# Optimization experiments

Hardware: AMD Instinct MI355X
Metric: run time of the kernel (lower is better)

## Reference

```python
import jax, jax.numpy as jnp
import numpy as np
import math

KORD = 3          # Chebyshev order K
N = 512           # num_of_vertices
D = 64            # d_model // 2
DM = 128          # d_model
NEG_SLOPE = 0.01  # torch F.leaky_relu default


def _cheb_coef_matrix(K):
    # coe[i] = 2/(K+1) * sum_j relu(temp)[j] * T_i(x_j), x_j = cos((K-j+0.5)pi/(K+1))
    xs = [math.cos((K - j + 0.5) * math.pi / (K + 1)) for j in range(K + 1)]
    M = np.array([[math.cos(i * math.acos(xj)) for xj in xs] for i in range(K + 1)],
                 dtype=np.float32)
    return (2.0 / (K + 1)) * M


def setup_inputs() -> dict:
    key = jax.random.key(0)
    ks = jax.random.split(key, 12)
    B, L = 4, 32
    sc_n = 1.0 / math.sqrt(N)
    sc_d = 1.0 / math.sqrt(D)
    return {
        "x":    jax.random.normal(ks[0], (B, L, N), jnp.float32),
        "adj":  jax.random.normal(ks[1], (N, N), jnp.float32) * sc_n,
        "Wp":   jax.random.normal(ks[2], (1, D), jnp.float32),            # project: Linear(1, D)
        "bp":   jnp.zeros((D,), jnp.float32),
        "Ksa":  jax.random.normal(ks[3], (N, N), jnp.float32) * sc_n,     # Spatial_Attention.K
        "Vsa":  jax.random.normal(ks[4], (N, N), jnp.float32) * sc_n,     # Spatial_Attention.V
        "bsa":  jax.random.normal(ks[5], (1, N, N), jnp.float32) * sc_n,  # Spatial_Attention.b
        "temp": jnp.ones((KORD + 1,), jnp.float32),                       # init fill_(1.0)
        "W1":   jax.random.normal(ks[6], (D, D), jnp.float32) * sc_d,     # Theta1_
        "b1":   jnp.zeros((D,), jnp.float32),
        "Wl":   jax.random.normal(ks[7], (N * D, DM), jnp.float32) / math.sqrt(N * D),  # linear_
        "bl":   jnp.zeros((DM,), jnp.float32),
    }


def _leaky(v):
    return jnp.where(v >= 0, v, NEG_SLOPE * v)


def reference(x, adj, Wp, bp, Ksa, Vsa, bsa, temp, W1, b1, Wl, bl):
    B, L, _ = x.shape
    # project: (B,L,N,1) @ (1,D) + bias -> (B,L,N,D)   (dropout = eval identity)
    h = x[..., None] * Wp[0] + bp

    # Chebyshev coefficients from relu(temp)
    coe = jnp.asarray(_cheb_coef_matrix(KORD)) @ jax.nn.relu(temp)  # (K+1,)

    # Chebyshev recursion on graph: Tx_{k+1} = 2*adj@Tx_k - Tx_{k-1}
    Tx0 = h
    Tx1 = jnp.einsum('nm,blmd->blnd', adj, h)
    A_x = coe[0] / 2 * Tx0 + coe[1] * Tx1
    for i in range(2, KORD + 1):
        Tx2 = 2 * jnp.einsum('nm,blmd->blnd', adj, Tx1) - Tx0
        A_x = A_x + coe[i] * Tx2
        Tx0, Tx1 = Tx1, Tx2

    # Spatial attention: softmax(V @ tanh(x (Kx)^T + b))
    Kx = jnp.einsum('nm,blmd->blnd', Ksa, h)                 # K @ x
    product = jnp.einsum('blnd,blmd->blnm', h, Kx)           # x @ (Kx)^T
    score = jnp.einsum('nm,blmc->blnc', Vsa, jnp.tanh(product + bsa[0]))
    SA = jax.nn.softmax(score, axis=-1)                      # (B,L,N,N)

    S_x = jnp.einsum('blnm,blmd->blnd', SA, h)
    g = A_x + S_x
    g = _leaky(jnp.einsum('blnd,de->blne', g, W1) + b1)      # Theta1_ + leaky_relu
    g = g.reshape(B, L, N * D)
    return _leaky(g @ Wl + bl)                               # linear_ + leaky_relu -> (B,L,DM)
```

## Files before the change

kernel.cpp:

```cpp
#include <hip/hip_runtime.h>
#include <math.h>

#define KORD 3
#ifndef M_PI
#define M_PI 3.14159265358979323846
#endif

typedef __attribute__((ext_vector_type(8))) __bf16 bf16x8;
typedef __attribute__((ext_vector_type(4))) float  f32x4;

__device__ __forceinline__ float leaky_(float v){ return v >= 0.f ? v : 0.01f*v; }

__device__ __forceinline__ float tanh_fast(float x){
  float xc = fminf(fmaxf(x, -10.f), 10.f);
  float t = __expf(2.f*xc);
  return (t - 1.f) * __builtin_amdgcn_rcpf(t + 1.f);
}

__device__ __forceinline__ f32x4 mfma16(bf16x8 a, bf16x8 b, f32x4 c){
  return __builtin_amdgcn_mfma_f32_16x16x32_bf16(a, b, c, 0, 0, 0);
}

__device__ __forceinline__ void gll16(const __bf16* g, __bf16* l){
  __builtin_amdgcn_global_load_lds(
      (__attribute__((address_space(1))) void*)(g),
      (__attribute__((address_space(3))) void*)(l), 16, 0, 0);
}

__global__ void k_coe(const float* __restrict__ temp, float* __restrict__ coe){
  if (threadIdx.x == 0 && blockIdx.x == 0){
    for (int i = 0; i <= KORD; ++i){
      float acc = 0.f;
      for (int j = 0; j <= KORD; ++j){
        double th = ((double)(KORD - j) + 0.5) * M_PI / (double)(KORD + 1);
        float t = temp[j]; t = t > 0.f ? t : 0.f;
        acc += t * (float)cos((double)i * th);
      }
      acc *= 2.f / (float)(KORD + 1);
      if (i >= 1 && fabsf(acc) < 1e-6f) acc = 0.f;
      coe[i] = acc;
    }
  }
}

__global__ __launch_bounds__(256) void k_cvt(const float* __restrict__ in,
                                             __bf16* __restrict__ out, int n){
  int i = blockIdx.x*256 + threadIdx.x;
  if (i < n) out[i] = (__bf16)in[i];
}

__global__ __launch_bounds__(256) void k_cvt_swz(const float* __restrict__ in,
                                                 __bf16* __restrict__ out){
  int i = blockIdx.x*256 + threadIdx.x;
  int r = i >> 9, c = i & 511;
  out[(size_t)r*512 + (c ^ ((r & 7) << 3))] = (__bf16)in[i];
}

__global__ __launch_bounds__(256) void k_w1t(const float* __restrict__ W1,
                                             __bf16* __restrict__ W1t){
  int t = threadIdx.x;
  for (int i = 0; i < 16; ++i){
    int e4 = i*256 + t;
    int e = e4 >> 6, d = e4 & 63;
    W1t[e*64 + d] = (__bf16)W1[d*64 + e];
  }
}

__global__ __launch_bounds__(256) void k_wlt(const float* __restrict__ Wl,
                                             __bf16* __restrict__ Wlt){
  __shared__ float Ls[64][65];
  int k0 = blockIdx.x*64, o0 = blockIdx.y*64;
  int t = threadIdx.x;
  for (int i = 0; i < 16; ++i){
    int e = i*256 + t; int r = e >> 6, c = e & 63;
    Ls[r][c] = Wl[(size_t)(k0 + r)*128 + o0 + c];
  }
  __syncthreads();
  for (int i = 0; i < 16; ++i){
    int e = i*256 + t; int r = e >> 6, c = e & 63;
    Wlt[(size_t)(o0 + r)*32768 + k0 + c] = (__bf16)Ls[c][r];
  }
}

__global__ __launch_bounds__(256) void k_bsat(const float* __restrict__ bsa,
                                              __bf16* __restrict__ bsaTb){
  __shared__ float Ls[64][65];
  int n0 = blockIdx.x*64, m0 = blockIdx.y*64;
  int t = threadIdx.x;
  for (int i = 0; i < 16; ++i){
    int e = i*256 + t; int r = e >> 6, c = e & 63;
    Ls[r][c] = bsa[(size_t)(n0 + r)*512 + m0 + c];
  }
  __syncthreads();
  for (int i = 0; i < 16; ++i){
    int e = i*256 + t; int r = e >> 6, c = e & 63;
    bsaTb[(size_t)(m0 + r)*512 + n0 + c] = (__bf16)Ls[c][r];
  }
}

__global__ __launch_bounds__(256) void k_embed2(const float* __restrict__ x,
    const float* __restrict__ Wp, const float* __restrict__ bp,
    __bf16* __restrict__ Ht, __bf16* __restrict__ Hnd, __bf16* __restrict__ Htsw){
  __shared__ float Ls[64][65];
  int cs = blockIdx.x, n0 = blockIdx.y*64;
  int t = threadIdx.x;
  for (int i = 0; i < 16; ++i){
    int e = i*256 + t; int d = e >> 6, nn = e & 63;
    float v = x[cs*512 + n0 + nn]*Wp[d] + bp[d];
    Ls[d][nn] = v;
    Ht[(size_t)(cs*64 + d)*512 + n0 + nn] = (__bf16)v;
    Htsw[(size_t)(cs*64 + d)*512 + ((n0 + nn) ^ ((d & 7) << 3))] = (__bf16)v;
  }
  __syncthreads();
  for (int i = 0; i < 16; ++i){
    int e = i*256 + t; int nn = e >> 6, d = e & 63;
    Hnd[((size_t)cs*512 + n0 + nn)*64 + d] = (__bf16)Ls[d][nn];
  }
}

__global__ __launch_bounds__(256) void k_combo(const __bf16* __restrict__ Ht,
    const __bf16* __restrict__ T1t, const __bf16* __restrict__ T2t,
    const __bf16* __restrict__ T3t, const __bf16* __restrict__ SXnd,
    const float* __restrict__ coe, __bf16* __restrict__ Gnd){
  __shared__ float Ls[64][65];
  int cs = blockIdx.x, n0 = blockIdx.y*64;
  int t = threadIdx.x;
  float c0 = coe[0]*0.5f, c1 = coe[1], c2 = coe[2], c3 = coe[3];
  for (int i = 0; i < 16; ++i){
    int e = i*256 + t; int d = e >> 6, nn = e & 63;
    size_t idx = (size_t)(cs*64 + d)*512 + n0 + nn;
    float v = c0*(float)Ht[idx];
    if (c1 != 0.f) v += c1*(float)T1t[idx];
    if (c2 != 0.f) v += c2*(float)T2t[idx];
    if (c3 != 0.f) v += c3*(float)T3t[idx];
    Ls[d][nn] = v;
  }
  __syncthreads();
  for (int i = 0; i < 16; ++i){
    int e = i*256 + t; int nn = e >> 6, d = e & 63;
    size_t oidx = ((size_t)cs*512 + n0 + nn)*64 + d;
    Gnd[oidx] = (__bf16)(Ls[d][nn] + (float)SXnd[oidx]);
  }
}

template<int BM, int BN, int WM, int WN, int EPI, bool SWZ>
__global__ __launch_bounds__(256) void gbt(
    const __bf16* __restrict__ A, size_t aB, int lda,
    const __bf16* __restrict__ B, size_t bB, int ldb,
    const void*  __restrict__ E, size_t eB,
    void* __restrict__ C, size_t cB, int ldc, int K, int gx, int gy,
    const float* __restrict__ gate, int gateCnt){
  if (gate){
    bool anyNZ = false;
    for (int i = 0; i < gateCnt; ++i) anyNZ |= (gate[i] != 0.f);
    if (!anyNZ) return;
  }
  constexpr int WTM = BM/WM, WTN = BN/WN;
  constexpr int FM = WTM/16, FN = WTN/16;
  constexpr int LDK = 72;
  constexpr bool RPK = (EPI == 2 && BM == 128 && BN == 128);
  __shared__ __bf16 SMEM[BM*LDK + BN*LDK];
  __bf16* As = SMEM;
  __bf16* Bs = SMEM + BM*LDK;
  const int tid = threadIdx.x;
  const int wave = tid >> 6, lane = tid & 63;
  const int wm = wave % WM, wn = wave / WM;
  int bx, by, bz;
  if (SWZ){
    int id = blockIdx.x;
    int xcd = id & 7, j = id >> 3;
    int tiles = gx*gy;
    int tile = j % tiles, sin = j / tiles;
    bz = xcd + 8*sin; bx = tile % gx; by = tile / gx;
  } else { bx = blockIdx.x; by = blockIdx.y; bz = blockIdx.z; }
  const int m0 = bx*BM, n0 = by*BN;
  const __bf16* Ab = A + (size_t)bz*aB + (size_t)m0*lda;
  const __bf16* Bb = B + (size_t)bz*bB + (size_t)n0*ldb;
  f32x4 acc[FM][FN] = {};
  for (int k0 = 0; k0 < K; k0 += 64){
    __syncthreads();
    constexpr int AIT = BM*64/(256*8);
#pragma unroll
    for (int i = 0; i < AIT; ++i){
      int e = i*256 + tid; int r = e >> 3, c = (e & 7)*8;
      *(float4*)&As[r*LDK + c] = *(const float4*)&Ab[(size_t)r*lda + k0 + c];
    }
    constexpr int BIT = BN*64/(256*8);
#pragma unroll
    for (int i = 0; i < BIT; ++i){
      int e = i*256 + tid; int r = e >> 3, c = (e & 7)*8;
      *(float4*)&Bs[r*LDK + c] = *(const float4*)&Bb[(size_t)r*ldb + k0 + c];
    }
    __syncthreads();
#pragma unroll
    for (int ks = 0; ks < 2; ++ks){
      bf16x8 af[FM], bfr[FN];
      const int ko = ks*32 + (lane >> 4)*8;
#pragma unroll
      for (int i = 0; i < FM; ++i)
        af[i] = *(const bf16x8*)&As[(wm*WTM + i*16 + (lane & 15))*LDK + ko];
#pragma unroll
      for (int j = 0; j < FN; ++j)
        bfr[j] = *(const bf16x8*)&Bs[(wn*WTN + j*16 + (lane & 15))*LDK + ko];
#pragma unroll
      for (int i = 0; i < FM; ++i)
#pragma unroll
        for (int j = 0; j < FN; ++j)
          acc[i][j] = mfma16(af[i], bfr[j], acc[i][j]);
    }
  }
  const int lr = (lane >> 4)*4, lc = lane & 15;
  __bf16* Cb = (__bf16*)C + (size_t)bz*cB;
  if constexpr (RPK){
    const __bf16* Eb = (const __bf16*)E;
    __syncthreads();
    __bf16* R = SMEM;
#pragma unroll
    for (int i = 0; i < FM; ++i)
#pragma unroll
      for (int j = 0; j < FN; ++j)
#pragma unroll
        for (int r = 0; r < 4; ++r){
          int row = wm*64 + i*16 + lr + r;
          int col = wn*64 + j*16 + lc;
          float v = tanh_fast(acc[i][j][r] + (float)Eb[(size_t)(m0 + row)*512 + (n0 + col)]);
          R[row*136 + col] = (__bf16)v;
        }
    __syncthreads();
#pragma unroll
    for (int it = 0; it < 8; ++it){
      int q = it*256 + tid; int row = q >> 4, ch = q & 15;
      *(bf16x8*)&Cb[(size_t)(m0 + row)*ldc + (n0 + ((ch*8) ^ ((row & 7) << 3)))] =
          *(const bf16x8*)&R[row*136 + ch*8];
    }
    return;
  }
  float*  Cf = (float*)C  + (size_t)bz*cB;
  const __bf16* Zb = (const __bf16*)E + (size_t)bz*eB;
  const float*  Ef = (const float*)E;
  const __bf16* Eb = (const __bf16*)E;
#pragma unroll
  for (int i = 0; i < FM; ++i){
    int row = m0 + wm*WTM + i*16 + lr;
#pragma unroll
    for (int j = 0; j < FN; ++j){
      int col = n0 + wn*WTN + j*16 + lc;
#pragma unroll
      for (int r = 0; r < 4; ++r){
        float v = acc[i][j][r];
        size_t idx = (size_t)(row + r)*ldc + col;
        if (EPI == 0){ Cb[idx] = (__bf16)v; }
        else if (EPI == 1){ Cb[idx] = (__bf16)(2.f*v - (float)Zb[idx]); }
        else if (EPI == 2){ Cb[(size_t)(row + r)*ldc + (col ^ (((row + r) & 7) << 3))] =
                              (__bf16)tanh_fast(v + (float)Eb[(size_t)(row + r)*512 + col]); }
        else if (EPI == 3){ Cf[idx] = v; }
        else if (EPI == 5){ float tt = v + Ef[col]; Cb[idx] = (__bf16)(tt >= 0.f ? tt : 0.01f*tt); }
      }
    }
  }
}

template<bool SWZ>
__global__ __launch_bounds__(256) void k_flash(
    const __bf16* __restrict__ Vsab,
    const __bf16* __restrict__ Pt,
    const __bf16* __restrict__ Htsw,
    __bf16* __restrict__ SXnd){
  __shared__ __bf16 VaL[2][4096];
  __shared__ __bf16 PbL[2][4096];
  __shared__ __bf16 Ps[64*72];
  __shared__ __bf16 Hb[4096];
  __shared__ float rs2[2][64];
  const int tid = threadIdx.x, wave = tid >> 6, lane = tid & 63;
  const int wm = wave & 1, wn = wave >> 1;
  const int lr = (lane >> 4)*4, lc = lane & 15;
  int np0, z;
  if (SWZ){
    int id = blockIdx.x;
    int xcd = id & 7, j = id >> 3;
    int tile = j & 7, sin = j >> 3;
    z = xcd + 8*sin; np0 = tile*64;
  } else { np0 = blockIdx.x*64; z = blockIdx.y; }
  const __bf16* Vb = Vsab + (size_t)np0*512;
  const __bf16* Pz = Pt + (size_t)z*262144;
  const __bf16* Hz = Htsw + (size_t)z*32768;
  const int srow = lane >> 3;
  const int scol = (lane & 7)*8;
  auto stage = [&](int buf, int c0, int k0){
#pragma unroll
    for (int rr = 0; rr < 2; ++rr){
      int rb = (rr*4 + wave)*8;
      gll16(Vb + (size_t)(rb + srow)*512 + k0 + scol, &VaL[buf][(rr*4 + wave)*512]);
      gll16(Pz + (size_t)(c0 + rb + srow)*512 + k0 + scol, &PbL[buf][(rr*4 + wave)*512]);
    }
  };
  const int kx = (lc & 7) << 3;
  f32x4 acc_sx[2][2] = {};
  float rowp[8] = {};
  stage(0, 0, 0);
  __syncthreads();
  for (int c0i = 0; c0i < 8; ++c0i){
    const int c0 = c0i*64;
    f32x4 acc_s[2][2] = {};
    for (int k0i = 0; k0i < 8; ++k0i){
      const int t = c0i*8 + k0i;
      const int cur = t & 1;
      if (t < 63){
        int nt = t + 1;
        stage(cur ^ 1, (nt >> 3)*64, (nt & 7)*64);
      }
      if (k0i == 1){
#pragma unroll
        for (int rr = 0; rr < 2; ++rr){
          int rb = (rr*4 + wave)*8;
          gll16(Hz + (size_t)(rb + srow)*512 + c0 + scol, &Hb[(rr*4 + wave)*512]);
        }
      }
#pragma unroll
      for (int ks = 0; ks < 2; ++ks){
        const int kox = (ks*32 + (lane >> 4)*8) ^ kx;
        bf16x8 a0 = *(const bf16x8*)&VaL[cur][(wm*32 +  0 + lc)*64 + kox];
        bf16x8 a1 = *(const bf16x8*)&VaL[cur][(wm*32 + 16 + lc)*64 + kox];
        bf16x8 b0 = *(const bf16x8*)&PbL[cur][(wn*32 +  0 + lc)*64 + kox];
        bf16x8 b1 = *(const bf16x8*)&PbL[cur][(wn*32 + 16 + lc)*64 + kox];
        acc_s[0][0] = mfma16(a0, b0, acc_s[0][0]);
        acc_s[0][1] = mfma16(a0, b1, acc_s[0][1]);
        acc_s[1][0] = mfma16(a1, b0, acc_s[1][0]);
        acc_s[1][1] = mfma16(a1, b1, acc_s[1][1]);
      }
      __syncthreads();
    }
#pragma unroll
    for (int i = 0; i < 2; ++i)
#pragma unroll
      for (int j = 0; j < 2; ++j)
#pragma unroll
        for (int rr = 0; rr < 4; ++rr){
          float e = __expf(fminf(acc_s[i][j][rr], 30.f));
          rowp[i*4 + rr] += e;
          Ps[(wm*32 + i*16 + lr + rr)*72 + wn*32 + j*16 + lc] = (__bf16)e;
        }
    __syncthreads();
#pragma unroll
    for (int ks = 0; ks < 2; ++ks){
      const int ko = ks*32 + (lane >> 4)*8;
      const int kox = ko ^ kx;
      bf16x8 p0 = *(const bf16x8*)&Ps[(wm*32 +  0 + lc)*72 + ko];
      bf16x8 p1 = *(const bf16x8*)&Ps[(wm*32 + 16 + lc)*72 + ko];
      bf16x8 h0 = *(const bf16x8*)&Hb[(wn*32 +  0 + lc)*64 + kox];
      bf16x8 h1 = *(const bf16x8*)&Hb[(wn*32 + 16 + lc)*64 + kox];
      acc_sx[0][0] = mfma16(p0, h0, acc_sx[0][0]);
      acc_sx[0][1] = mfma16(p0, h1, acc_sx[0][1]);
      acc_sx[1][0] = mfma16(p1, h0, acc_sx[1][0]);
      acc_sx[1][1] = mfma16(p1, h1, acc_sx[1][1]);
    }
  }
#pragma unroll
  for (int s = 0; s < 8; ++s){
    float v = rowp[s];
    v += __shfl_xor(v, 1, 64); v += __shfl_xor(v, 2, 64);
    v += __shfl_xor(v, 4, 64); v += __shfl_xor(v, 8, 64);
    rowp[s] = v;
  }
  __syncthreads();
  if ((lane & 15) == 0){
#pragma unroll
    for (int i = 0; i < 2; ++i)
#pragma unroll
      for (int rr = 0; rr < 4; ++rr)
        rs2[wn][wm*32 + i*16 + lr + rr] = rowp[i*4 + rr];
  }
  __syncthreads();
#pragma unroll
  for (int i = 0; i < 2; ++i)
#pragma unroll
    for (int rr = 0; rr < 4; ++rr){
      int row = wm*32 + i*16 + lr + rr;
      float inv = __builtin_amdgcn_rcpf(rs2[0][row] + rs2[1][row]);
#pragma unroll
      for (int j = 0; j < 2; ++j){
        int col = wn*32 + j*16 + lc;
        SXnd[((size_t)z*512 + np0 + row)*64 + col] = (__bf16)(acc_sx[i][j][rr]*inv);
      }
    }
}

__global__ __launch_bounds__(256) void k_final2(
    const float* __restrict__ part, const float* __restrict__ bl,
    float* __restrict__ out){
  int idx = blockIdx.x*256 + threadIdx.x;
  int o = idx & 127;
  float acc = bl[o];
#pragma unroll 8
  for (int p = 0; p < 128; ++p) acc += part[(size_t)p*16384 + idx];
  out[idx] = leaky_(acc);
}

extern "C" void kernel_launch(void* const* d_in, const int* in_sizes, int n_in,
                              void* d_out, int out_size, void* d_ws, size_t ws_size,
                              hipStream_t stream){
  const float* x    = (const float*)d_in[0];
  const float* adj  = (const float*)d_in[1];
  const float* Wp   = (const float*)d_in[2];
  const float* bp   = (const float*)d_in[3];
  const float* Ksa  = (const float*)d_in[4];
  const float* Vsa  = (const float*)d_in[5];
  const float* bsa  = (const float*)d_in[6];
  const float* temp = (const float*)d_in[7];
  const float* W1   = (const float*)d_in[8];
  const float* b1   = (const float*)d_in[9];
  const float* Wl   = (const float*)d_in[10];
  const float* bl   = (const float*)d_in[11];
  float* out = (float*)d_out;

  char* ws = (char*)d_ws;
  size_t off = 0;
  auto alloc = [&](size_t bytes){ void* p = ws + off; off += (bytes + 255) & ~(size_t)255; return p; };
  float*  coe  = (float*)alloc(64);
  __bf16* G2b  = (__bf16*)alloc((size_t)128*32768*2);
  __bf16* Wlt  = (__bf16*)alloc((size_t)128*32768*2);
  float*  part = (float*)alloc((size_t)128*16384*4);
  __bf16* bsaTb= (__bf16*)alloc((size_t)512*512*2);
  __bf16* adjb = (__bf16*)alloc((size_t)512*512*2);
  __bf16* Ksab = (__bf16*)alloc((size_t)512*512*2);
  __bf16* Vsab = (__bf16*)alloc((size_t)512*512*2);
  __bf16* W1t  = (__bf16*)alloc((size_t)64*64*2);
  const size_t fixedOff = off;

  int CH = 128;
  while (CH > 2){
    size_t need = fixedOff + (size_t)CH*(9*65536 + 524288) + 65536;
    if (need <= ws_size) break;
    CH >>= 1;
  }
  __bf16* Ht   = (__bf16*)alloc((size_t)CH*65536);
  __bf16* Htsw = (__bf16*)alloc((size_t)CH*65536);
  __bf16* T1t  = (__bf16*)alloc((size_t)CH*65536);
  __bf16* T2t  = (__bf16*)alloc((size_t)CH*65536);
  __bf16* T3t  = (__bf16*)alloc((size_t)CH*65536);
  __bf16* KXnd = (__bf16*)alloc((size_t)CH*65536);
  __bf16* Hnd  = (__bf16*)alloc((size_t)CH*65536);
  __bf16* SXnd = (__bf16*)alloc((size_t)CH*65536);
  __bf16* Gnd  = (__bf16*)alloc((size_t)CH*65536);
  __bf16* Pt   = (__bf16*)alloc((size_t)CH*524288);

  const bool swz = (CH % 8) == 0;

  k_coe<<<1, 64, 0, stream>>>(temp, coe);
  k_cvt<<<1024, 256, 0, stream>>>(adj, adjb, 512*512);
  k_cvt<<<1024, 256, 0, stream>>>(Ksa, Ksab, 512*512);
  k_cvt_swz<<<1024, 256, 0, stream>>>(Vsa, Vsab);
  k_w1t<<<1, 256, 0, stream>>>(W1, W1t);
  k_wlt<<<dim3(512,2), 256, 0, stream>>>(Wl, Wlt);
  k_bsat<<<dim3(8,8), 256, 0, stream>>>(bsa, bsaTb);

  for (int s0 = 0; s0 < 128; s0 += CH){
    k_embed2<<<dim3(CH,8), 256, 0, stream>>>(x + (size_t)s0*512, Wp, bp, Ht, Hnd, Htsw);
    gbt<64,128,2,2,0,false><<<dim3(CH,4,1), 256, 0, stream>>>(Ht, 0, 512, adjb, 0, 512, nullptr, 0, T1t, 0, 512, 512, 0, 0, coe+1, 3);
    gbt<64,128,2,2,1,false><<<dim3(CH,4,1), 256, 0, stream>>>(T1t, 0, 512, adjb, 0, 512, Ht, 0, T2t, 0, 512, 512, 0, 0, coe+2, 2);
    gbt<64,128,2,2,1,false><<<dim3(CH,4,1), 256, 0, stream>>>(T2t, 0, 512, adjb, 0, 512, T1t, 0, T3t, 0, 512, 512, 0, 0, coe+3, 1);
    gbt<64,64,2,2,0,false><<<dim3(8,1,CH), 256, 0, stream>>>(Ksab, 0, 512, Ht, 32768, 512,
                                                             nullptr, 0, KXnd, 32768, 64, 512, 0, 0, nullptr, 0);
    if (swz)
      gbt<128,128,2,2,2,true><<<dim3(16*CH), 256, 0, stream>>>(KXnd, 32768, 64, Hnd, 32768, 64,
                                                               bsaTb, 0, Pt, 262144, 512, 64, 4, 4, nullptr, 0);
    else
      gbt<128,128,2,2,2,false><<<dim3(4,4,CH), 256, 0, stream>>>(KXnd, 32768, 64, Hnd, 32768, 64,
                                                                 bsaTb, 0, Pt, 262144, 512, 64, 0, 0, nullptr, 0);
    if (swz)
      k_flash<true><<<dim3(8*CH), 256, 0, stream>>>(Vsab, Pt, Htsw, SXnd);
    else
      k_flash<false><<<dim3(8,CH), 256, 0, stream>>>(Vsab, Pt, Htsw, SXnd);
    k_combo<<<dim3(CH,8), 256, 0, stream>>>(Ht, T1t, T2t, T3t, SXnd, coe, Gnd);
    gbt<64,64,2,2,5,false><<<dim3(8,1,CH), 256, 0, stream>>>(Gnd, 32768, 64, W1t, 0, 64,
                                                             b1, 0, G2b + (size_t)s0*32768, 32768, 64, 64, 0, 0, nullptr, 0);
  }

  gbt<128,128,2,2,3,false><<<dim3(1,1,128), 256, 0, stream>>>(G2b, 256, 32768, Wlt, 256, 32768,
                                                              nullptr, 0, part, 16384, 128, 256, 0, 0, nullptr, 0);
  k_final2<<<dim3(64), 256, 0, stream>>>(part, bl, out);
}
```

Baseline: 196.4 us.

## Triple-buffer flash kernel loads and read H directly from global memory

The flash kernel moves from double to triple buffering for the V and P tiles, keeping two stages in flight and using explicit vmcnt waits with a single barrier per step instead of __syncthreads. The H operand is now loaded straight from global memory into registers rather than staged through a swizzled LDS buffer. That lets the embed kernel drop the swizzled Htsw copy and frees one workspace buffer. In exchange it relies on hand-counted vmcnt values, which could race if the count of outstanding loads is wrong, and the H reads from global are uncoalesced.

```diff
diff --git a/kernel.cpp b/kernel.cpp
--- a/kernel.cpp
+++ b/kernel.cpp
@@ -100,7 +100,7 @@
 
 __global__ __launch_bounds__(256) void k_embed2(const float* __restrict__ x,
     const float* __restrict__ Wp, const float* __restrict__ bp,
-    __bf16* __restrict__ Ht, __bf16* __restrict__ Hnd, __bf16* __restrict__ Htsw){
+    __bf16* __restrict__ Ht, __bf16* __restrict__ Hnd){
   __shared__ float Ls[64][65];
   int cs = blockIdx.x, n0 = blockIdx.y*64;
   int t = threadIdx.x;
@@ -109,7 +109,6 @@
     float v = x[cs*512 + n0 + nn]*Wp[d] + bp[d];
     Ls[d][nn] = v;
     Ht[(size_t)(cs*64 + d)*512 + n0 + nn] = (__bf16)v;
-    Htsw[(size_t)(cs*64 + d)*512 + ((n0 + nn) ^ ((d & 7) << 3))] = (__bf16)v;
   }
   __syncthreads();
   for (int i = 0; i < 16; ++i){
@@ -264,12 +263,11 @@
 __global__ __launch_bounds__(256) void k_flash(
     const __bf16* __restrict__ Vsab,
     const __bf16* __restrict__ Pt,
-    const __bf16* __restrict__ Htsw,
+    const __bf16* __restrict__ Ht,
     __bf16* __restrict__ SXnd){
-  __shared__ __bf16 VaL[2][4096];
-  __shared__ __bf16 PbL[2][4096];
+  __shared__ __bf16 VaL[3][4096];
+  __shared__ __bf16 PbL[3][4096];
   __shared__ __bf16 Ps[64*72];
-  __shared__ __bf16 Hb[4096];
   __shared__ float rs2[2][64];
   const int tid = threadIdx.x, wave = tid >> 6, lane = tid & 63;
   const int wm = wave & 1, wn = wave >> 1;
@@ -283,10 +281,10 @@
   } else { np0 = blockIdx.x*64; z = blockIdx.y; }
   const __bf16* Vb = Vsab + (size_t)np0*512;
   const __bf16* Pz = Pt + (size_t)z*262144;
-  const __bf16* Hz = Htsw + (size_t)z*32768;
+  const __bf16* Hz = Ht + (size_t)z*32768;
   const int srow = lane >> 3;
   const int scol = (lane & 7)*8;
-  auto stage = [&](int buf, int c0, int k0){
+  auto stageVP = [&](int buf, int c0, int k0){
 #pragma unroll
     for (int rr = 0; rr < 2; ++rr){
       int rb = (rr*4 + wave)*8;
@@ -297,38 +295,41 @@
   const int kx = (lc & 7) << 3;
   f32x4 acc_sx[2][2] = {};
   float rowp[8] = {};
-  stage(0, 0, 0);
-  __syncthreads();
+  stageVP(0, 0, 0);
+  stageVP(1, 0, 64);
+  int cur = 0;
   for (int c0i = 0; c0i < 8; ++c0i){
     const int c0 = c0i*64;
     f32x4 acc_s[2][2] = {};
+#pragma unroll
     for (int k0i = 0; k0i < 8; ++k0i){
-      const int t = c0i*8 + k0i;
-      const int cur = t & 1;
-      if (t < 63){
-        int nt = t + 1;
-        stage(cur ^ 1, (nt >> 3)*64, (nt & 7)*64);
-      }
-      if (k0i == 1){
-#pragma unroll
-        for (int rr = 0; rr < 2; ++rr){
-          int rb = (rr*4 + wave)*8;
-          gll16(Hz + (size_t)(rb + srow)*512 + c0 + scol, &Hb[(rr*4 + wave)*512]);
-        }
-      }
+      if (k0i == 7){
+        if (c0i == 7) asm volatile("s_waitcnt vmcnt(0)" ::: "memory");
+        else          asm volatile("s_waitcnt vmcnt(4)" ::: "memory");
+      } else {
+        asm volatile("s_waitcnt vmcnt(4)" ::: "memory");
+      }
+      __builtin_amdgcn_s_barrier();
+      const __bf16* Vc = VaL[cur];
+      const __bf16* Pc = PbL[cur];
 #pragma unroll
       for (int ks = 0; ks < 2; ++ks){
         const int kox = (ks*32 + (lane >> 4)*8) ^ kx;
-        bf16x8 a0 = *(const bf16x8*)&VaL[cur][(wm*32 +  0 + lc)*64 + kox];
-        bf16x8 a1 = *(const bf16x8*)&VaL[cur][(wm*32 + 16 + lc)*64 + kox];
-        bf16x8 b0 = *(const bf16x8*)&PbL[cur][(wn*32 +  0 + lc)*64 + kox];
-        bf16x8 b1 = *(const bf16x8*)&PbL[cur][(wn*32 + 16 + lc)*64 + kox];
+        bf16x8 a0 = *(const bf16x8*)&Vc[(wm*32 +  0 + lc)*64 + kox];
+        bf16x8 a1 = *(const bf16x8*)&Vc[(wm*32 + 16 + lc)*64 + kox];
+        bf16x8 b0 = *(const bf16x8*)&Pc[(wn*32 +  0 + lc)*64 + kox];
+        bf16x8 b1 = *(const bf16x8*)&Pc[(wn*32 + 16 + lc)*64 + kox];
         acc_s[0][0] = mfma16(a0, b0, acc_s[0][0]);
         acc_s[0][1] = mfma16(a0, b1, acc_s[0][1]);
         acc_s[1][0] = mfma16(a1, b0, acc_s[1][0]);
         acc_s[1][1] = mfma16(a1, b1, acc_s[1][1]);
       }
-      __syncthreads();
+      int nt = c0i*8 + k0i + 2;
+      if (nt < 64){
+        int bufn = cur + 2; if (bufn >= 3) bufn -= 3;
+        stageVP(bufn, (nt >> 3) << 6, (nt & 7) << 6);
+      }
+      cur = (cur == 2) ? 0 : cur + 1;
     }
 #pragma unroll
     for (int i = 0; i < 2; ++i)
@@ -340,19 +341,24 @@
           rowp[i*4 + rr] += e;
           Ps[(wm*32 + i*16 + lr + rr)*72 + wn*32 + j*16 + lc] = (__bf16)e;
         }
-    __syncthreads();
+    bf16x8 h0k[2], h1k[2];
 #pragma unroll
     for (int ks = 0; ks < 2; ++ks){
       const int ko = ks*32 + (lane >> 4)*8;
-      const int kox = ko ^ kx;
+      h0k[ks] = *(const bf16x8*)&Hz[(size_t)(wn*32 +  0 + lc)*512 + c0 + ko];
+      h1k[ks] = *(const bf16x8*)&Hz[(size_t)(wn*32 + 16 + lc)*512 + c0 + ko];
+    }
+    asm volatile("s_waitcnt lgkmcnt(0)" ::: "memory");
+    __builtin_amdgcn_s_barrier();
+#pragma unroll
+    for (int ks = 0; ks < 2; ++ks){
+      const int ko = ks*32 + (lane >> 4)*8;
       bf16x8 p0 = *(const bf16x8*)&Ps[(wm*32 +  0 + lc)*72 + ko];
       bf16x8 p1 = *(const bf16x8*)&Ps[(wm*32 + 16 + lc)*72 + ko];
-      bf16x8 h0 = *(const bf16x8*)&Hb[(wn*32 +  0 + lc)*64 + kox];
-      bf16x8 h1 = *(const bf16x8*)&Hb[(wn*32 + 16 + lc)*64 + kox];
-      acc_sx[0][0] = mfma16(p0, h0, acc_sx[0][0]);
-      acc_sx[0][1] = mfma16(p0, h1, acc_sx[0][1]);
-      acc_sx[1][0] = mfma16(p1, h0, acc_sx[1][0]);
-      acc_sx[1][1] = mfma16(p1, h1, acc_sx[1][1]);
+      acc_sx[0][0] = mfma16(p0, h0k[ks], acc_sx[0][0]);
+      acc_sx[0][1] = mfma16(p0, h1k[ks], acc_sx[0][1]);
+      acc_sx[1][0] = mfma16(p1, h0k[ks], acc_sx[1][0]);
+      acc_sx[1][1] = mfma16(p1, h1k[ks], acc_sx[1][1]);
     }
   }
 #pragma unroll
@@ -429,12 +435,11 @@
 
   int CH = 128;
   while (CH > 2){
-    size_t need = fixedOff + (size_t)CH*(9*65536 + 524288) + 65536;
+    size_t need = fixedOff + (size_t)CH*(8*65536 + 524288) + 65536;
     if (need <= ws_size) break;
     CH >>= 1;
   }
   __bf16* Ht   = (__bf16*)alloc((size_t)CH*65536);
-  __bf16* Htsw = (__bf16*)alloc((size_t)CH*65536);
   __bf16* T1t  = (__bf16*)alloc((size_t)CH*65536);
   __bf16* T2t  = (__bf16*)alloc((size_t)CH*65536);
   __bf16* T3t  = (__bf16*)alloc((size_t)CH*65536);
@@ -455,7 +460,7 @@
   k_bsat<<<dim3(8,8), 256, 0, stream>>>(bsa, bsaTb);
 
   for (int s0 = 0; s0 < 128; s0 += CH){
-    k_embed2<<<dim3(CH,8), 256, 0, stream>>>(x + (size_t)s0*512, Wp, bp, Ht, Hnd, Htsw);
+    k_embed2<<<dim3(CH,8), 256, 0, stream>>>(x + (size_t)s0*512, Wp, bp, Ht, Hnd);
     gbt<64,128,2,2,0,false><<<dim3(CH,4,1), 256, 0, stream>>>(Ht, 0, 512, adjb, 0, 512, nullptr, 0, T1t, 0, 512, 512, 0, 0, coe+1, 3);
     gbt<64,128,2,2,1,false><<<dim3(CH,4,1), 256, 0, stream>>>(T1t, 0, 512, adjb, 0, 512, Ht, 0, T2t, 0, 512, 512, 0, 0, coe+2, 2);
     gbt<64,128,2,2,1,false><<<dim3(CH,4,1), 256, 0, stream>>>(T2t, 0, 512, adjb, 0, 512, T1t, 0, T3t, 0, 512, 512, 0, 0, coe+3, 1);
@@ -468,9 +473,9 @@
       gbt<128,128,2,2,2,false><<<dim3(4,4,CH), 256, 0, stream>>>(KXnd, 32768, 64, Hnd, 32768, 64,
                                                                  bsaTb, 0, Pt, 262144, 512, 64, 0, 0, nullptr, 0);
     if (swz)
-      k_flash<true><<<dim3(8*CH), 256, 0, stream>>>(Vsab, Pt, Htsw, SXnd);
+      k_flash<true><<<dim3(8*CH), 256, 0, stream>>>(Vsab, Pt, Ht, SXnd);
     else
-      k_flash<false><<<dim3(8,CH), 256, 0, stream>>>(Vsab, Pt, Htsw, SXnd);
+      k_flash<false><<<dim3(8,CH), 256, 0, stream>>>(Vsab, Pt, Ht, SXnd);
     k_combo<<<dim3(CH,8), 256, 0, stream>>>(Ht, T1t, T2t, T3t, SXnd, coe, Gnd);
     gbt<64,64,2,2,5,false><<<dim3(8,1,CH), 256, 0, stream>>>(Gnd, 32768, 64, W1t, 0, 64,
                                                              b1, 0, G2b + (size_t)s0*32768, 32768, 64, 64, 0, 0, nullptr, 0);
```

After: 187.6 us (median of 3 runs). 4.5% less time.
